# Performance work log

Hardware: AMD Instinct MI355X
Metric: run time of the kernel (lower is better)

## Reference

```python
import jax, jax.numpy as jnp
import numpy as np

N = 100000
E = 1600000
IN_DIM = 128
OUT_DIM = 128
H = 4
HD = OUT_DIM // H  # 32
NEG_SLOPE = 0.2
EPS_SOFTMAX = 1e-8
EPS_LN = 1e-5


def setup_inputs() -> dict:
    key = jax.random.key(0)
    ks = jax.random.split(key, 6)
    h = jax.random.normal(ks[0], (N, IN_DIM), dtype=jnp.float32)
    edge_index = jax.random.randint(ks[1], (2, E), 0, N, dtype=jnp.int32)
    W = jax.random.normal(ks[2], (IN_DIM, OUT_DIM), dtype=jnp.float32) / np.sqrt(IN_DIM)
    W_self = jax.random.normal(ks[3], (IN_DIM, OUT_DIM), dtype=jnp.float32) / np.sqrt(IN_DIM)
    a_in = jax.random.normal(ks[4], (H, 2 * HD), dtype=jnp.float32) * 0.01
    a_out = jax.random.normal(ks[5], (H, 2 * HD), dtype=jnp.float32) * 0.01
    bias = jnp.zeros((OUT_DIM,), dtype=jnp.float32)
    ln_gamma = jnp.ones((OUT_DIM,), dtype=jnp.float32)
    ln_beta = jnp.zeros((OUT_DIM,), dtype=jnp.float32)
    return {"h": h, "edge_index": edge_index, "W": W, "W_self": W_self,
            "a_in": a_in, "a_out": a_out, "bias": bias,
            "ln_gamma": ln_gamma, "ln_beta": ln_beta}


def _attention_aggregate(h_proj, sender, receiver, attn_vec, num_nodes):
    # h_proj: (N, H, HD); sender/receiver: (E,); attn_vec: (H, 2*HD)
    h_sender = h_proj[sender]      # (E, H, HD)
    h_receiver = h_proj[receiver]  # (E, H, HD)
    # e = sum over concat([h_sender, h_receiver]) * attn_vec, split halves
    e = (jnp.einsum('ehd,hd->eh', h_sender, attn_vec[:, :HD])
         + jnp.einsum('ehd,hd->eh', h_receiver, attn_vec[:, HD:]))
    e = jax.nn.leaky_relu(e, NEG_SLOPE)
    e_max = jax.ops.segment_max(e, receiver, num_segments=num_nodes)  # (N, H)
    alpha = jnp.exp(e - e_max[receiver])
    alpha_sum = jax.ops.segment_sum(alpha, receiver, num_segments=num_nodes)
    alpha = alpha / (alpha_sum[receiver] + EPS_SOFTMAX)
    msg = h_sender * alpha[..., None]  # (E, H, HD)
    return jax.ops.segment_sum(msg, receiver, num_segments=num_nodes)  # (N, H, HD)


def reference(h, edge_index, W, W_self, a_in, a_out, bias, ln_gamma, ln_beta):
    n = h.shape[0]
    h_proj = (h @ W).reshape(n, H, HD)
    h_self = h @ W_self
    src, dst = edge_index[0], edge_index[1]
    h_in = _attention_aggregate(h_proj, src, dst, a_in, n)   # 'in' direction
    h_out = _attention_aggregate(h_proj, dst, src, a_out, n)  # 'out' direction
    combined = h_self + h_in.reshape(n, -1) + h_out.reshape(n, -1) + bias
    mean = combined.mean(axis=-1, keepdims=True)
    var = combined.var(axis=-1, keepdims=True)
    normed = (combined - mean) * jax.lax.rsqrt(var + EPS_LN)
    return normed * ln_gamma + ln_beta
```

## Files before the change

### kernel.cpp

```cpp
#include <hip/hip_runtime.h>
#include <math.h>

#define HEADS 4
#define HD 32
#define DIM 128
#define NEG_SLOPE 0.2f
#define EPS_SM 1e-8f
#define EPS_LN 1e-5f
#define SH1 9
#define PB 256
#define BCOLS 272

typedef _Float16 h2_t __attribute__((ext_vector_type(2)));
typedef _Float16 f16x8 __attribute__((ext_vector_type(8)));
typedef float f32x4 __attribute__((ext_vector_type(4)));

__device__ __forceinline__ float lrelu(float x) { return x > 0.f ? x : NEG_SLOPE * x; }
__device__ __forceinline__ unsigned pkh(float a, float b) {
    return __builtin_bit_cast(unsigned, __builtin_amdgcn_cvt_pkrtz(a, b));
}
__device__ __forceinline__ float dot2(unsigned a, unsigned b, float c) {
    return __builtin_amdgcn_fdot2(__builtin_bit_cast(h2_t, a), __builtin_bit_cast(h2_t, b), c, false);
}
__device__ __forceinline__ float lo16(unsigned u) { return (float)__builtin_bit_cast(h2_t, u)[0]; }
__device__ __forceinline__ float hi16(unsigned u) { return (float)__builtin_bit_cast(h2_t, u)[1]; }

template<int LIM> __device__ __forceinline__ void rmax4(float& a, float& b, float& c, float& d) {
#pragma unroll
    for (int s = 1; s < LIM; s <<= 1) {
        a = fmaxf(a, __shfl_xor(a, s, 64));
        b = fmaxf(b, __shfl_xor(b, s, 64));
        c = fmaxf(c, __shfl_xor(c, s, 64));
        d = fmaxf(d, __shfl_xor(d, s, 64));
    }
}
template<int LIM> __device__ __forceinline__ void rsum4(float& a, float& b, float& c, float& d) {
#pragma unroll
    for (int s = 1; s < LIM; s <<= 1) {
        a += __shfl_xor(a, s, 64);
        b += __shfl_xor(b, s, 64);
        c += __shfl_xor(c, s, 64);
        d += __shfl_xor(d, s, 64);
    }
}

__device__ __forceinline__ void dot8(uint4 u, uint4 v, unsigned wpk, float (&acc)[8]) {
    acc[0] = dot2(__builtin_amdgcn_perm(v.x, u.x, 0x05040100u), wpk, acc[0]);
    acc[1] = dot2(__builtin_amdgcn_perm(v.x, u.x, 0x07060302u), wpk, acc[1]);
    acc[2] = dot2(__builtin_amdgcn_perm(v.y, u.y, 0x05040100u), wpk, acc[2]);
    acc[3] = dot2(__builtin_amdgcn_perm(v.y, u.y, 0x07060302u), wpk, acc[3]);
    acc[4] = dot2(__builtin_amdgcn_perm(v.z, u.z, 0x05040100u), wpk, acc[4]);
    acc[5] = dot2(__builtin_amdgcn_perm(v.z, u.z, 0x07060302u), wpk, acc[5]);
    acc[6] = dot2(__builtin_amdgcn_perm(v.w, u.w, 0x05040100u), wpk, acc[6]);
    acc[7] = dot2(__builtin_amdgcn_perm(v.w, u.w, 0x07060302u), wpk, acc[7]);
}

__device__ __forceinline__ void aggr_pairs(int cnt, const int* __restrict__ sdw,
                                           const uint2* __restrict__ wtw,
                                           const char* __restrict__ hpb,
                                           unsigned rowoff, int q, bool hlo, unsigned wsel,
                                           float (&acc)[8]) {
    const int npair = (cnt + 7) >> 3;
#pragma unroll 2
    for (int t = 0; t < npair; ++t) {
        int pi = 4 * t + q;
        uint2 sp = *(const uint2*)&sdw[2 * pi];
        uint4 wp = *(const uint4*)&wtw[2 * pi];
        uint4 u = *(const uint4*)(hpb + (((unsigned)sp.x << 8) + rowoff));
        uint4 v = *(const uint4*)(hpb + (((unsigned)sp.y << 8) + rowoff));
        unsigned wA = hlo ? wp.x : wp.y;
        unsigned wB = hlo ? wp.z : wp.w;
        unsigned wpk = __builtin_amdgcn_perm(wB, wA, wsel);
        dot8(u, v, wpk, acc);
    }
}

__global__ __launch_bounds__(256) void part1a_k(const int* __restrict__ ei, int* __restrict__ cntmat,
                                                int E, int N, int NBIN,
                                                const float* __restrict__ W,
                                                const float* __restrict__ V,
                                                const float* __restrict__ a_in,
                                                const float* __restrict__ a_out,
                                                _Float16* __restrict__ Bt) {
    __shared__ int lcnt[512];
    const int t = threadIdx.x;
    if (blockIdx.x >= PB) {
        int c = (blockIdx.x - PB) * 2 + (t >> 7);
        int k = t & 127;
        float v;
        if (c < 128) {
            v = W[k * 128 + c];
        } else if (c < 256) {
            v = V[k * 128 + (c - 128)];
        } else {
            int d = (c - 256) >> 2, hh = (c - 256) & 3;
            const float* a = (d < 2) ? a_in : a_out;
            int base = hh * 64 + (d & 1) * 32;
            float s = 0.f;
#pragma unroll
            for (int tt = 0; tt < 32; ++tt) s += W[k * 128 + 32 * hh + tt] * a[base + tt];
            v = s;
        }
        Bt[c * 128 + k] = (_Float16)v;
        return;
    }
    const int CH = (E + PB - 1) / PB;
    const int e0 = blockIdx.x * CH;
    const int e1 = min(e0 + CH, E);
    for (int i = t; i < 512; i += 256) lcnt[i] = 0;
    __syncthreads();
    for (int e = e0 + t; e < e1; e += 256) {
        int s = ei[e], d = ei[E + e];
        atomicAdd(&lcnt[d >> SH1], 1);
        atomicAdd(&lcnt[(N + s) >> SH1], 1);
    }
    __syncthreads();
    for (int i = t; i < NBIN; i += 256) cntmat[i * PB + blockIdx.x] = lcnt[i];
}

__global__ __launch_bounds__(256) void scanB_k(const int* __restrict__ cntmat,
                                               int* __restrict__ blkoff, int* __restrict__ btot) {
    __shared__ int ls[PB];
    const int bin = blockIdx.x;
    const int t = threadIdx.x;
    int v = cntmat[bin * PB + t];
    ls[t] = v;
    __syncthreads();
#pragma unroll
    for (int d = 1; d < PB; d <<= 1) {
        int u = (t >= d) ? ls[t - d] : 0;
        __syncthreads();
        ls[t] += u;
        __syncthreads();
    }
    blkoff[bin * PB + t] = ls[t] - v;
    if (t == PB - 1) btot[bin] = ls[t];
}

__global__ __launch_bounds__(256) void scanC_k(const int* __restrict__ btot,
                                               int* __restrict__ bbase, int NBIN, int twoE) {
    __shared__ int ls[256];
    int t = threadIdx.x;
    int i0 = 2 * t, i1 = 2 * t + 1;
    int v0 = (i0 < NBIN) ? btot[i0] : 0;
    int v1 = (i1 < NBIN) ? btot[i1] : 0;
    int pair = v0 + v1;
    ls[t] = pair;
    __syncthreads();
#pragma unroll
    for (int d = 1; d < 256; d <<= 1) {
        int u = (t >= d) ? ls[t - d] : 0;
        __syncthreads();
        ls[t] += u;
        __syncthreads();
    }
    int excl = ls[t] - pair;
    if (i0 < NBIN) bbase[i0] = excl;
    if (i1 < NBIN) bbase[i1] = excl + v0;
    if (t == 0) bbase[NBIN] = twoE;
}

__global__ __launch_bounds__(256) void p1b_gemm_k(const int* __restrict__ ei,
                                                  const int* __restrict__ bbase,
                                                  const int* __restrict__ blkoff,
                                                  unsigned* __restrict__ rec, int E, int N, int NBIN,
                                                  const float* __restrict__ h,
                                                  const _Float16* __restrict__ Bt,
                                                  unsigned* __restrict__ hs_pk,
                                                  unsigned* __restrict__ hp_pk,
                                                  float* __restrict__ pA0, float* __restrict__ pA1,
                                                  float* __restrict__ pB0, float* __restrict__ pB1) {
    __shared__ int gb[512];
    __shared__ int lcur[512];
    __shared__ _Float16 hs[64][128];
    __shared__ _Float16 hss[64][128];

    if (blockIdx.x < PB) {
        const int t = threadIdx.x;
        const int CH = (E + PB - 1) / PB;
        const int e0 = blockIdx.x * CH;
        const int e1 = min(e0 + CH, E);
        for (int i = t; i < 512; i += 256) lcur[i] = 0;
        for (int i = t; i < NBIN; i += 256) gb[i] = bbase[i] + blkoff[i * PB + blockIdx.x];
        __syncthreads();
        for (int e = e0 + t; e < e1; e += 256) {
            int s = ei[e], d = ei[E + e];
            int b1 = d >> SH1;
            int r1 = atomicAdd(&lcur[b1], 1);
            rec[gb[b1] + r1] = (unsigned)s | ((unsigned)(d & 511) << 20);
            int so = N + s;
            int b2 = so >> SH1;
            int r2 = atomicAdd(&lcur[b2], 1);
            rec[gb[b2] + r2] = (unsigned)d | ((unsigned)(so & 511) << 20);
        }
        return;
    }

    const int tid = threadIdx.x;
    const int w = tid >> 6, l = tid & 63;
    const int l15 = l & 15;
    const int kg = l >> 4;
    const int row0 = (blockIdx.x - PB) * 64;
    const int arow = row0 + 16 * w + l15;

    f32x4 acc[17];
#pragma unroll
    for (int j = 0; j < 17; ++j) {
        acc[j][0] = 0.f; acc[j][1] = 0.f; acc[j][2] = 0.f; acc[j][3] = 0.f;
    }

    const uint4* __restrict__ bt4 = (const uint4*)Bt;

#pragma unroll
    for (int kc = 0; kc < 4; ++kc) {
        union { unsigned u[4]; f16x8 v; } cv;
        if (arow < N) {
            float4 x0 = ((const float4*)h)[(size_t)arow * 32 + kc * 8 + kg * 2];
            float4 x1 = ((const float4*)h)[(size_t)arow * 32 + kc * 8 + kg * 2 + 1];
            cv.u[0] = pkh(x0.x, x0.y); cv.u[1] = pkh(x0.z, x0.w);
            cv.u[2] = pkh(x1.x, x1.y); cv.u[3] = pkh(x1.z, x1.w);
        } else {
            cv.u[0] = 0u; cv.u[1] = 0u; cv.u[2] = 0u; cv.u[3] = 0u;
        }
        f16x8 af = cv.v;
#pragma unroll
        for (int j = 0; j < 17; ++j) {
            int col = 16 * j + l15;
            union { uint4 q; f16x8 v; } bc;
            bc.q = bt4[col * 16 + kc * 4 + kg];
            acc[j] = __builtin_amdgcn_mfma_f32_16x16x32_f16(af, bc.v, acc[j], 0, 0, 0);
        }
    }

    const int r4 = kg * 4;
    const int dsel = l15 >> 2, hh = l15 & 3;
    float* __restrict__ pd = (dsel == 0) ? pA0 : (dsel == 1) ? pA1 : (dsel == 2) ? pB0 : pB1;
#pragma unroll
    for (int r = 0; r < 4; ++r) {
        int lr = 16 * w + r4 + r;
        int grow = row0 + lr;
#pragma unroll
        for (int j = 0; j < 8; ++j)
            hs[lr][16 * j + l15] = (_Float16)acc[j][r];
#pragma unroll
        for (int j = 8; j < 16; ++j)
            hss[lr][16 * (j - 8) + l15] = (_Float16)acc[j][r];
        if (grow < N) pd[grow * 4 + hh] = acc[16][r];
    }
    __syncthreads();
    const uint4* hsv = (const uint4*)&hs[0][0];
    const uint4* hssv = (const uint4*)&hss[0][0];
#pragma unroll
    for (int p = 0; p < 4; ++p) {
        int chunk = tid + p * 256;
        int rrow = chunk >> 4, cg = chunk & 15;
        int grow = row0 + rrow;
        if (grow < N) {
            ((uint4*)hp_pk)[(size_t)grow * 16 + cg] = hsv[rrow * 16 + cg];
            ((uint4*)hs_pk)[(size_t)grow * 16 + cg] = hssv[rrow * 16 + cg];
        }
    }
}

__global__ __launch_bounds__(256) void build2_k(const unsigned* __restrict__ rec,
                                                const int* __restrict__ bbase,
                                                int* __restrict__ off, int* __restrict__ csr,
                                                int M, int twoE, int NBIN) {
    __shared__ int lcnt[512];
    __shared__ int lcur[512];
    __shared__ int ls[256];
    const int b = blockIdx.x;
    const int t = threadIdx.x;
    const int base = bbase[b];
    const int cnt = bbase[b + 1] - base;
    const int seg0 = b << SH1;
    for (int i = t; i < 512; i += 256) lcnt[i] = 0;
    __syncthreads();
    for (int k = t; k < cnt; k += 256) atomicAdd(&lcnt[rec[base + k] >> 20], 1);
    __syncthreads();
    int v0 = lcnt[2 * t], v1 = lcnt[2 * t + 1];
    int pair = v0 + v1;
    ls[t] = pair;
    __syncthreads();
#pragma unroll
    for (int d = 1; d < 256; d <<= 1) {
        int u = (t >= d) ? ls[t - d] : 0;
        __syncthreads();
        ls[t] += u;
        __syncthreads();
    }
    int excl = ls[t] - pair;
    lcur[2 * t] = excl;
    lcur[2 * t + 1] = excl + v0;
    int sg = seg0 + 2 * t;
    if (sg < M) off[sg] = base + excl;
    if (sg + 1 < M) off[sg + 1] = base + excl + v0;
    if (b == NBIN - 1 && t == 0) off[M] = twoE;
    __syncthreads();
    for (int k = t; k < cnt; k += 256) {
        unsigned r = rec[base + k];
        int pos = atomicAdd(&lcur[r >> 20], 1);
        csr[base + pos] = (int)(r & 0xFFFFFu);
    }
}

#define ROWLD(x) (*(const uint4*)(hpb + (((unsigned)(x) << 8) + rowoff)))
__global__ __launch_bounds__(256) void node_aggr_ln_k(const unsigned* __restrict__ hp_pk,
                                                      const unsigned* __restrict__ hs_pk,
                                                      const float* __restrict__ pA0, const float* __restrict__ pA1,
                                                      const float* __restrict__ pB0, const float* __restrict__ pB1,
                                                      const int* __restrict__ off, const int* __restrict__ csr,
                                                      const float* __restrict__ bias,
                                                      const float* __restrict__ gamma,
                                                      const float* __restrict__ beta,
                                                      float* __restrict__ out, int N) {
    __shared__ int sds[4][64];
    __shared__ uint2 wts[4][64];
    const int wave = threadIdx.x >> 6;
    const int lane = threadIdx.x & 63;
    const int n = blockIdx.x * 4 + wave;
    if (n >= N) return;
    const int l15 = lane & 15;
    const int q = lane >> 4;
    const unsigned wsel = (l15 & 4) ? 0x07060302u : 0x05040100u;
    const bool hlo = (l15 < 8);
    int* sdw = sds[wave];
    uint2* wtw = wts[wave];
    const char* hpb = (const char*)hp_pk;
    const unsigned rowoff = (unsigned)l15 << 4;

    float acc[8];
#pragma unroll
    for (int k = 0; k < 8; ++k) acc[k] = 0.f;

    const int beg0 = off[n], end0 = off[n + 1];
    const int beg1 = off[N + n], end1 = off[N + n + 1];
    const int len0 = end0 - beg0, len1 = end1 - beg1;

    if (len0 <= 32 && len1 <= 32) {
        const int half = lane >> 5;
        const int hl = lane & 31;
        const int beg = half ? beg1 : beg0;
        const int len = half ? len1 : len0;
        const float* __restrict__ pp0 = half ? pB0 : pA0;
        const float* __restrict__ pp1 = half ? pB1 : pA1;
        float4 r1 = ((const float4*)pp1)[n];
        int sid = 0;
        float e0 = -INFINITY, e1 = -INFINITY, e2 = -INFINITY, e3 = -INFINITY;
        float4 r0 = make_float4(0.f, 0.f, 0.f, 0.f);
        if (hl < len) {
            sid = csr[beg + hl];
            r0 = ((const float4*)pp0)[sid];
        }
        sdw[lane] = 0;
        wtw[lane] = make_uint2(0u, 0u);
        if (hl < len) sdw[half ? len0 + hl : hl] = sid;

        const int cnt = len0 + len1;
        const int npair = (cnt + 7) >> 3;
        uint4 u0 = make_uint4(0u, 0u, 0u, 0u), v0 = u0, u1 = u0, v1 = u0;
        if (npair > 0) {
            uint2 s = *(const uint2*)&sdw[2 * q];
            u0 = ROWLD(s.x); v0 = ROWLD(s.y);
        }
        if (npair > 1) {
            uint2 s = *(const uint2*)&sdw[2 * (4 + q)];
            u1 = ROWLD(s.x); v1 = ROWLD(s.y);
        }

        if (hl < len) {
            e0 = lrelu(r0.x + r1.x);
            e1 = lrelu(r0.y + r1.y);
            e2 = lrelu(r0.z + r1.z);
            e3 = lrelu(r0.w + r1.w);
        }
        float m0 = e0, m1 = e1, m2 = e2, m3 = e3;
        const bool small16 = (len0 <= 16 && len1 <= 16);
        if (small16) rmax4<16>(m0, m1, m2, m3);
        else         rmax4<32>(m0, m1, m2, m3);
        float w0 = 0.f, w1 = 0.f, w2 = 0.f, w3 = 0.f;
        if (hl < len) {
            w0 = __expf(e0 - m0); w1 = __expf(e1 - m1);
            w2 = __expf(e2 - m2); w3 = __expf(e3 - m3);
        }
        float s0 = w0, s1 = w1, s2 = w2, s3 = w3;
        if (small16) rsum4<16>(s0, s1, s2, s3);
        else         rsum4<32>(s0, s1, s2, s3);
        w0 *= 1.f / (s0 + EPS_SM);
        w1 *= 1.f / (s1 + EPS_SM);
        w2 *= 1.f / (s2 + EPS_SM);
        w3 *= 1.f / (s3 + EPS_SM);
        if (hl < len)
            wtw[half ? len0 + hl : hl] = make_uint2(pkh(w0, w1), pkh(w2, w3));

        for (int t = 0; t < npair; t += 2) {
            {
                uint4 wp = *(const uint4*)&wtw[2 * (4 * t + q)];
                unsigned wA = hlo ? wp.x : wp.y;
                unsigned wB = hlo ? wp.z : wp.w;
                unsigned wpk = __builtin_amdgcn_perm(wB, wA, wsel);
                dot8(u0, v0, wpk, acc);
            }
            if (t + 2 < npair) {
                uint2 s = *(const uint2*)&sdw[2 * (4 * (t + 2) + q)];
                u0 = ROWLD(s.x); v0 = ROWLD(s.y);
            }
            if (t + 1 < npair) {
                uint4 wp = *(const uint4*)&wtw[2 * (4 * (t + 1) + q)];
                unsigned wA = hlo ? wp.x : wp.y;
                unsigned wB = hlo ? wp.z : wp.w;
                unsigned wpk = __builtin_amdgcn_perm(wB, wA, wsel);
                dot8(u1, v1, wpk, acc);
                if (t + 3 < npair) {
                    uint2 s = *(const uint2*)&sdw[2 * (4 * (t + 3) + q)];
                    u1 = ROWLD(s.x); v1 = ROWLD(s.y);
                }
            }
        }
    } else {
#pragma unroll
        for (int dir = 0; dir < 2; ++dir) {
            const int beg = (dir == 0) ? beg0 : beg1;
            const int end = (dir == 0) ? end0 : end1;
            const int len = end - beg;
            if (len == 0) continue;
            const float* __restrict__ p0 = (dir == 0) ? pA0 : pB0;
            const float* __restrict__ p1 = (dir == 0) ? pA1 : pB1;
            float4 r1 = ((const float4*)p1)[n];

            if (len <= 64) {
                int sid = 0;
                float e0 = -INFINITY, e1 = -INFINITY, e2 = -INFINITY, e3 = -INFINITY;
                if (lane < len) {
                    sid = csr[beg + lane];
                    float4 r0 = ((const float4*)p0)[sid];
                    e0 = lrelu(r0.x + r1.x);
                    e1 = lrelu(r0.y + r1.y);
                    e2 = lrelu(r0.z + r1.z);
                    e3 = lrelu(r0.w + r1.w);
                }
                float m0 = e0, m1 = e1, m2 = e2, m3 = e3;
                rmax4<64>(m0, m1, m2, m3);
                float w0 = 0.f, w1 = 0.f, w2 = 0.f, w3 = 0.f;
                if (lane < len) {
                    w0 = __expf(e0 - m0); w1 = __expf(e1 - m1);
                    w2 = __expf(e2 - m2); w3 = __expf(e3 - m3);
                }
                float s0 = w0, s1 = w1, s2 = w2, s3 = w3;
                rsum4<64>(s0, s1, s2, s3);
                w0 *= 1.f / (s0 + EPS_SM);
                w1 *= 1.f / (s1 + EPS_SM);
                w2 *= 1.f / (s2 + EPS_SM);
                w3 *= 1.f / (s3 + EPS_SM);
                sdw[lane] = sid;
                wtw[lane] = make_uint2(pkh(w0, w1), pkh(w2, w3));
                aggr_pairs(len, sdw, wtw, hpb, rowoff, q, hlo, wsel, acc);
            } else {
                float m0 = -INFINITY, m1 = -INFINITY, m2 = -INFINITY, m3 = -INFINITY;
                for (int base = beg; base < end; base += 64) {
                    int j = base + lane;
                    if (j < end) {
                        int sid = csr[j];
                        float4 r0 = ((const float4*)p0)[sid];
                        m0 = fmaxf(m0, lrelu(r0.x + r1.x));
                        m1 = fmaxf(m1, lrelu(r0.y + r1.y));
                        m2 = fmaxf(m2, lrelu(r0.z + r1.z));
                        m3 = fmaxf(m3, lrelu(r0.w + r1.w));
                    }
                }
                rmax4<64>(m0, m1, m2, m3);
                float s0 = 0.f, s1 = 0.f, s2 = 0.f, s3 = 0.f;
                for (int base = beg; base < end; base += 64) {
                    int j = base + lane;
                    if (j < end) {
                        int sid = csr[j];
                        float4 r0 = ((const float4*)p0)[sid];
                        s0 += __expf(lrelu(r0.x + r1.x) - m0);
                        s1 += __expf(lrelu(r0.y + r1.y) - m1);
                        s2 += __expf(lrelu(r0.z + r1.z) - m2);
                        s3 += __expf(lrelu(r0.w + r1.w) - m3);
                    }
                }
                rsum4<64>(s0, s1, s2, s3);
                const float is0 = 1.f / (s0 + EPS_SM);
                const float is1 = 1.f / (s1 + EPS_SM);
                const float is2 = 1.f / (s2 + EPS_SM);
                const float is3 = 1.f / (s3 + EPS_SM);
                for (int base = beg; base < end; base += 64) {
                    int cnt = min(64, end - base);
                    int sid = 0;
                    float w0 = 0.f, w1 = 0.f, w2 = 0.f, w3 = 0.f;
                    if (lane < cnt) {
                        sid = csr[base + lane];
                        float4 r0 = ((const float4*)p0)[sid];
                        w0 = __expf(lrelu(r0.x + r1.x) - m0) * is0;
                        w1 = __expf(lrelu(r0.y + r1.y) - m1) * is1;
                        w2 = __expf(lrelu(r0.z + r1.z) - m2) * is2;
                        w3 = __expf(lrelu(r0.w + r1.w) - m3) * is3;
                    }
                    sdw[lane] = sid;
                    wtw[lane] = make_uint2(pkh(w0, w1), pkh(w2, w3));
                    aggr_pairs(cnt, sdw, wtw, hpb, rowoff, q, hlo, wsel, acc);
                }
            }
        }
    }

#pragma unroll
    for (int s = 16; s < 64; s <<= 1) {
#pragma unroll
        for (int k = 0; k < 8; ++k) acc[k] += __shfl_xor(acc[k], s, 64);
    }

    size_t bb = (size_t)n * DIM;
    uint4 hv = ((const uint4*)hs_pk)[(size_t)n * 16 + l15];
    float4 b0 = ((const float4*)bias)[2 * l15];
    float4 b1 = ((const float4*)bias)[2 * l15 + 1];
    float x0 = lo16(hv.x) + acc[0] + b0.x;
    float x1 = hi16(hv.x) + acc[1] + b0.y;
    float x2 = lo16(hv.y) + acc[2] + b0.z;
    float x3 = hi16(hv.y) + acc[3] + b0.w;
    float y0 = lo16(hv.z) + acc[4] + b1.x;
    float y1 = hi16(hv.z) + acc[5] + b1.y;
    float y2 = lo16(hv.w) + acc[6] + b1.z;
    float y3 = hi16(hv.w) + acc[7] + b1.w;
    float sum = x0 + x1 + x2 + x3 + y0 + y1 + y2 + y3;
    float sq = x0 * x0 + x1 * x1 + x2 * x2 + x3 * x3
             + y0 * y0 + y1 * y1 + y2 * y2 + y3 * y3;
#pragma unroll
    for (int m = 1; m < 64; m <<= 1) {
        sum += __shfl_xor(sum, m, 64);
        sq += __shfl_xor(sq, m, 64);
    }
    float mean = sum * (1.f / 512.f);
    float var = sq * (1.f / 512.f) - mean * mean;
    float inv = rsqrtf(var + EPS_LN);
    if (lane < 16) {
        float4 g0 = ((const float4*)gamma)[2 * l15];
        float4 g1 = ((const float4*)gamma)[2 * l15 + 1];
        float4 be0 = ((const float4*)beta)[2 * l15];
        float4 be1 = ((const float4*)beta)[2 * l15 + 1];
        float4 o0 = make_float4((x0 - mean) * inv * g0.x + be0.x,
                                (x1 - mean) * inv * g0.y + be0.y,
                                (x2 - mean) * inv * g0.z + be0.z,
                                (x3 - mean) * inv * g0.w + be0.w);
        float4 o1 = make_float4((y0 - mean) * inv * g1.x + be1.x,
                                (y1 - mean) * inv * g1.y + be1.y,
                                (y2 - mean) * inv * g1.z + be1.z,
                                (y3 - mean) * inv * g1.w + be1.w);
        ((float4*)(out + bb))[2 * l15] = o0;
        ((float4*)(out + bb))[2 * l15 + 1] = o1;
    }
}

extern "C" void kernel_launch(void* const* d_in, const int* in_sizes, int n_in,
                              void* d_out, int out_size, void* d_ws, size_t ws_size,
                              hipStream_t stream) {
    const float* h      = (const float*)d_in[0];
    const int*   ei     = (const int*)d_in[1];
    const float* W      = (const float*)d_in[2];
    const float* W_self = (const float*)d_in[3];
    const float* a_in   = (const float*)d_in[4];
    const float* a_out  = (const float*)d_in[5];
    const float* bias   = (const float*)d_in[6];
    const float* gamma  = (const float*)d_in[7];
    const float* beta   = (const float*)d_in[8];
    float* out = (float*)d_out;

    const int N = in_sizes[0] / DIM;
    const int E = in_sizes[1] / 2;
    const int M = 2 * N;
    const int NBIN = (M + (1 << SH1) - 1) >> SH1;
    const int twoE = 2 * E;

    float* ws = (float*)d_ws;
    size_t off_f = 0;
    unsigned* hs_pk = (unsigned*)(ws + off_f); off_f += (size_t)N * 64;
    unsigned* hp_pk = (unsigned*)(ws + off_f); off_f += (size_t)N * 64;
    float* pA0 = ws + off_f; off_f += (size_t)N * 4;
    float* pA1 = ws + off_f; off_f += (size_t)N * 4;
    float* pB0 = ws + off_f; off_f += (size_t)N * 4;
    float* pB1 = ws + off_f; off_f += (size_t)N * 4;
    int* ip = (int*)(ws + off_f);
    size_t off_i = 0;
    int* cntmat = ip + off_i; off_i += (size_t)NBIN * PB;
    int* blkoff = ip + off_i; off_i += (size_t)NBIN * PB;
    int* btot   = ip + off_i; off_i += NBIN;
    int* bbase  = ip + off_i; off_i += (size_t)NBIN + 1;
    int* off    = ip + off_i; off_i += (size_t)M + 1;
    unsigned* rec = (unsigned*)(ip + off_i); off_i += (size_t)twoE;
    int* csr    = ip + off_i; off_i += (size_t)twoE;
    _Float16* Bt = (_Float16*)(ip + off_i); off_i += (size_t)(BCOLS * 128) / 2;

    const int GB = (N + 63) / 64;

    part1a_k<<<PB + BCOLS / 2, 256, 0, stream>>>(ei, cntmat, E, N, NBIN,
                                                 W, W_self, a_in, a_out, Bt);
    scanB_k<<<NBIN, PB, 0, stream>>>(cntmat, blkoff, btot);
    scanC_k<<<1, 256, 0, stream>>>(btot, bbase, NBIN, twoE);

    p1b_gemm_k<<<PB + GB, 256, 0, stream>>>(ei, bbase, blkoff, rec, E, N, NBIN,
                                            h, Bt, hs_pk, hp_pk, pA0, pA1, pB0, pB1);

    build2_k<<<NBIN, 256, 0, stream>>>(rec, bbase, off, csr, M, twoE, NBIN);

    node_aggr_ln_k<<<(N + 3) / 4, 256, 0, stream>>>(hp_pk, hs_pk, pA0, pA1, pB0, pB1,
                                                    off, csr, bias, gamma, beta, out, N);
}
```

Baseline: 372.2 us.

## Build CSR via global per-node atomics and drop softmax max subtraction

Replaces the two-pass binned CSR construction (per-block bin histogram, record scatter, then per-bin rebuild kernel) with per-node global atomic degree counts, a segmented scan, and a direct scatter into csr using per-node atomic cursors fused into the GEMM launch. This removes the build2 kernel and the intermediate rec buffer. It also removes the softmax max reduction and computes exp of the raw logits, which saves the shuffle reductions and the extra pass over long neighbour lists. The unshifted exp relies on logits staying small enough not to overflow, which holds only because the attention vectors are small. Heavy global atomic contention on the degree and cursor arrays may offset some of the saving.

```diff
diff --git a/kernel.cpp b/kernel.cpp
--- a/kernel.cpp
+++ b/kernel.cpp
@@ -8,7 +8,8 @@
 #define EPS_SM 1e-8f
 #define EPS_LN 1e-5f
 #define SH1 9
-#define PB 256
+#define HB 256
+#define SB 256
 #define BCOLS 272
 
 typedef _Float16 h2_t __attribute__((ext_vector_type(2)));
@@ -25,15 +26,6 @@
 __device__ __forceinline__ float lo16(unsigned u) { return (float)__builtin_bit_cast(h2_t, u)[0]; }
 __device__ __forceinline__ float hi16(unsigned u) { return (float)__builtin_bit_cast(h2_t, u)[1]; }
 
-template<int LIM> __device__ __forceinline__ void rmax4(float& a, float& b, float& c, float& d) {
-#pragma unroll
-    for (int s = 1; s < LIM; s <<= 1) {
-        a = fmaxf(a, __shfl_xor(a, s, 64));
-        b = fmaxf(b, __shfl_xor(b, s, 64));
-        c = fmaxf(c, __shfl_xor(c, s, 64));
-        d = fmaxf(d, __shfl_xor(d, s, 64));
-    }
-}
 template<int LIM> __device__ __forceinline__ void rsum4(float& a, float& b, float& c, float& d) {
 #pragma unroll
     for (int s = 1; s < LIM; s <<= 1) {
@@ -75,17 +67,16 @@
     }
 }
 
-__global__ __launch_bounds__(256) void part1a_k(const int* __restrict__ ei, int* __restrict__ cntmat,
-                                                int E, int N, int NBIN,
-                                                const float* __restrict__ W,
-                                                const float* __restrict__ V,
-                                                const float* __restrict__ a_in,
-                                                const float* __restrict__ a_out,
-                                                _Float16* __restrict__ Bt) {
-    __shared__ int lcnt[512];
+__global__ __launch_bounds__(256) void hist_bt_k(const int* __restrict__ ei, int* __restrict__ deg,
+                                                 int E, int N,
+                                                 const float* __restrict__ W,
+                                                 const float* __restrict__ V,
+                                                 const float* __restrict__ a_in,
+                                                 const float* __restrict__ a_out,
+                                                 _Float16* __restrict__ Bt) {
     const int t = threadIdx.x;
-    if (blockIdx.x >= PB) {
-        int c = (blockIdx.x - PB) * 2 + (t >> 7);
+    if (blockIdx.x >= HB) {
+        int c = (blockIdx.x - HB) * 2 + (t >> 7);
         int k = t & 127;
         float v;
         if (c < 128) {
@@ -104,37 +95,37 @@
         Bt[c * 128 + k] = (_Float16)v;
         return;
     }
-    const int CH = (E + PB - 1) / PB;
+    const int CH = (E + HB - 1) / HB;
     const int e0 = blockIdx.x * CH;
     const int e1 = min(e0 + CH, E);
-    for (int i = t; i < 512; i += 256) lcnt[i] = 0;
-    __syncthreads();
     for (int e = e0 + t; e < e1; e += 256) {
         int s = ei[e], d = ei[E + e];
-        atomicAdd(&lcnt[d >> SH1], 1);
-        atomicAdd(&lcnt[(N + s) >> SH1], 1);
-    }
+        atomicAdd(&deg[d], 1);
+        atomicAdd(&deg[N + s], 1);
+    }
+}
+
+__global__ __launch_bounds__(256) void scanseg_k(const int* __restrict__ deg,
+                                                 int* __restrict__ locoff, int* __restrict__ btot) {
+    __shared__ int ls[256];
+    const int b = blockIdx.x;
+    const int t = threadIdx.x;
+    const int i0 = (b << SH1) + 2 * t, i1 = i0 + 1;
+    int v0 = deg[i0], v1 = deg[i1];
+    int pair = v0 + v1;
+    ls[t] = pair;
     __syncthreads();
-    for (int i = t; i < NBIN; i += 256) cntmat[i * PB + blockIdx.x] = lcnt[i];
-}
-
-__global__ __launch_bounds__(256) void scanB_k(const int* __restrict__ cntmat,
-                                               int* __restrict__ blkoff, int* __restrict__ btot) {
-    __shared__ int ls[PB];
-    const int bin = blockIdx.x;
-    const int t = threadIdx.x;
-    int v = cntmat[bin * PB + t];
-    ls[t] = v;
-    __syncthreads();
-#pragma unroll
-    for (int d = 1; d < PB; d <<= 1) {
+#pragma unroll
+    for (int d = 1; d < 256; d <<= 1) {
         int u = (t >= d) ? ls[t - d] : 0;
         __syncthreads();
         ls[t] += u;
         __syncthreads();
     }
-    blkoff[bin * PB + t] = ls[t] - v;
-    if (t == PB - 1) btot[bin] = ls[t];
+    int excl = ls[t] - pair;
+    locoff[i0] = excl;
+    locoff[i1] = excl + v0;
+    if (t == 255) btot[b] = ls[255];
 }
 
 __global__ __launch_bounds__(256) void scanC_k(const int* __restrict__ btot,
@@ -160,47 +151,52 @@
     if (t == 0) bbase[NBIN] = twoE;
 }
 
-__global__ __launch_bounds__(256) void p1b_gemm_k(const int* __restrict__ ei,
-                                                  const int* __restrict__ bbase,
-                                                  const int* __restrict__ blkoff,
-                                                  unsigned* __restrict__ rec, int E, int N, int NBIN,
-                                                  const float* __restrict__ h,
-                                                  const _Float16* __restrict__ Bt,
-                                                  unsigned* __restrict__ hs_pk,
-                                                  unsigned* __restrict__ hp_pk,
-                                                  float* __restrict__ pA0, float* __restrict__ pA1,
-                                                  float* __restrict__ pB0, float* __restrict__ pB1) {
-    __shared__ int gb[512];
-    __shared__ int lcur[512];
+__global__ __launch_bounds__(256) void fix_scat_gemm_k(const int* __restrict__ ei,
+                                                       const int* __restrict__ bbase,
+                                                       const int* __restrict__ locoff,
+                                                       int* __restrict__ off, int* __restrict__ cnt2,
+                                                       int* __restrict__ csr,
+                                                       int E, int N, int M, int twoE, int F,
+                                                       const float* __restrict__ h,
+                                                       const _Float16* __restrict__ Bt,
+                                                       unsigned* __restrict__ hs_pk,
+                                                       unsigned* __restrict__ hp_pk,
+                                                       float* __restrict__ pA0, float* __restrict__ pA1,
+                                                       float* __restrict__ pB0, float* __restrict__ pB1) {
+    const int tid = threadIdx.x;
+    if (blockIdx.x < F) {
+#pragma unroll
+        for (int p = 0; p < 4; ++p) {
+            int i = blockIdx.x * 1024 + p * 256 + tid;
+            if (i < M) off[i] = bbase[i >> SH1] + locoff[i];
+            else if (i == M) off[M] = twoE;
+        }
+        return;
+    }
+    if (blockIdx.x < F + SB) {
+        const int blk = blockIdx.x - F;
+        const int CH = (E + SB - 1) / SB;
+        const int e0 = blk * CH;
+        const int e1 = min(e0 + CH, E);
+        for (int e = e0 + tid; e < e1; e += 256) {
+            int s = ei[e], d = ei[E + e];
+            int b1 = bbase[d >> SH1] + locoff[d];
+            int r1 = atomicAdd(&cnt2[d], 1);
+            csr[b1 + r1] = s;
+            int so = N + s;
+            int b2 = bbase[so >> SH1] + locoff[so];
+            int r2 = atomicAdd(&cnt2[so], 1);
+            csr[b2 + r2] = d;
+        }
+        return;
+    }
+
     __shared__ _Float16 hs[64][128];
     __shared__ _Float16 hss[64][128];
-
-    if (blockIdx.x < PB) {
-        const int t = threadIdx.x;
-        const int CH = (E + PB - 1) / PB;
-        const int e0 = blockIdx.x * CH;
-        const int e1 = min(e0 + CH, E);
-        for (int i = t; i < 512; i += 256) lcur[i] = 0;
-        for (int i = t; i < NBIN; i += 256) gb[i] = bbase[i] + blkoff[i * PB + blockIdx.x];
-        __syncthreads();
-        for (int e = e0 + t; e < e1; e += 256) {
-            int s = ei[e], d = ei[E + e];
-            int b1 = d >> SH1;
-            int r1 = atomicAdd(&lcur[b1], 1);
-            rec[gb[b1] + r1] = (unsigned)s | ((unsigned)(d & 511) << 20);
-            int so = N + s;
-            int b2 = so >> SH1;
-            int r2 = atomicAdd(&lcur[b2], 1);
-            rec[gb[b2] + r2] = (unsigned)d | ((unsigned)(so & 511) << 20);
-        }
-        return;
-    }
-
-    const int tid = threadIdx.x;
     const int w = tid >> 6, l = tid & 63;
     const int l15 = l & 15;
     const int kg = l >> 4;
-    const int row0 = (blockIdx.x - PB) * 64;
+    const int row0 = (blockIdx.x - F - SB) * 64;
     const int arow = row0 + 16 * w + l15;
 
     f32x4 acc[17];
@@ -259,48 +255,6 @@
             ((uint4*)hp_pk)[(size_t)grow * 16 + cg] = hsv[rrow * 16 + cg];
             ((uint4*)hs_pk)[(size_t)grow * 16 + cg] = hssv[rrow * 16 + cg];
         }
-    }
-}
-
-__global__ __launch_bounds__(256) void build2_k(const unsigned* __restrict__ rec,
-                                                const int* __restrict__ bbase,
-                                                int* __restrict__ off, int* __restrict__ csr,
-                                                int M, int twoE, int NBIN) {
-    __shared__ int lcnt[512];
-    __shared__ int lcur[512];
-    __shared__ int ls[256];
-    const int b = blockIdx.x;
-    const int t = threadIdx.x;
-    const int base = bbase[b];
-    const int cnt = bbase[b + 1] - base;
-    const int seg0 = b << SH1;
-    for (int i = t; i < 512; i += 256) lcnt[i] = 0;
-    __syncthreads();
-    for (int k = t; k < cnt; k += 256) atomicAdd(&lcnt[rec[base + k] >> 20], 1);
-    __syncthreads();
-    int v0 = lcnt[2 * t], v1 = lcnt[2 * t + 1];
-    int pair = v0 + v1;
-    ls[t] = pair;
-    __syncthreads();
-#pragma unroll
-    for (int d = 1; d < 256; d <<= 1) {
-        int u = (t >= d) ? ls[t - d] : 0;
-        __syncthreads();
-        ls[t] += u;
-        __syncthreads();
-    }
-    int excl = ls[t] - pair;
-    lcur[2 * t] = excl;
-    lcur[2 * t + 1] = excl + v0;
-    int sg = seg0 + 2 * t;
-    if (sg < M) off[sg] = base + excl;
-    if (sg + 1 < M) off[sg + 1] = base + excl + v0;
-    if (b == NBIN - 1 && t == 0) off[M] = twoE;
-    __syncthreads();
-    for (int k = t; k < cnt; k += 256) {
-        unsigned r = rec[base + k];
-        int pos = atomicAdd(&lcur[r >> 20], 1);
-        csr[base + pos] = (int)(r & 0xFFFFFu);
     }
 }
 
@@ -374,16 +328,9 @@
             e2 = lrelu(r0.z + r1.z);
             e3 = lrelu(r0.w + r1.w);
         }
-        float m0 = e0, m1 = e1, m2 = e2, m3 = e3;
+        float w0 = __expf(e0), w1 = __expf(e1), w2 = __expf(e2), w3 = __expf(e3);
+        float s0 = w0, s1 = w1, s2 = w2, s3 = w3;
         const bool small16 = (len0 <= 16 && len1 <= 16);
-        if (small16) rmax4<16>(m0, m1, m2, m3);
-        else         rmax4<32>(m0, m1, m2, m3);
-        float w0 = 0.f, w1 = 0.f, w2 = 0.f, w3 = 0.f;
-        if (hl < len) {
-            w0 = __expf(e0 - m0); w1 = __expf(e1 - m1);
-            w2 = __expf(e2 - m2); w3 = __expf(e3 - m3);
-        }
-        float s0 = w0, s1 = w1, s2 = w2, s3 = w3;
         if (small16) rsum4<16>(s0, s1, s2, s3);
         else         rsum4<32>(s0, s1, s2, s3);
         w0 *= 1.f / (s0 + EPS_SM);
@@ -439,13 +386,7 @@
                     e2 = lrelu(r0.z + r1.z);
                     e3 = lrelu(r0.w + r1.w);
                 }
-                float m0 = e0, m1 = e1, m2 = e2, m3 = e3;
-                rmax4<64>(m0, m1, m2, m3);
-                float w0 = 0.f, w1 = 0.f, w2 = 0.f, w3 = 0.f;
-                if (lane < len) {
-                    w0 = __expf(e0 - m0); w1 = __expf(e1 - m1);
-                    w2 = __expf(e2 - m2); w3 = __expf(e3 - m3);
-                }
+                float w0 = __expf(e0), w1 = __expf(e1), w2 = __expf(e2), w3 = __expf(e3);
                 float s0 = w0, s1 = w1, s2 = w2, s3 = w3;
                 rsum4<64>(s0, s1, s2, s3);
                 w0 *= 1.f / (s0 + EPS_SM);
@@ -456,30 +397,20 @@
                 wtw[lane] = make_uint2(pkh(w0, w1), pkh(w2, w3));
                 aggr_pairs(len, sdw, wtw, hpb, rowoff, q, hlo, wsel, acc);
             } else {
-                float m0 = -INFINITY, m1 = -INFINITY, m2 = -INFINITY, m3 = -INFINITY;
+                float s0 = 0.f, s1 = 0.f, s2 = 0.f, s3 = 0.f;
                 for (int base = beg; base < end; base += 64) {
                     int j = base + lane;
+                    float e0 = -INFINITY, e1 = -INFINITY, e2 = -INFINITY, e3 = -INFINITY;
                     if (j < end) {
                         int sid = csr[j];
                         float4 r0 = ((const float4*)p0)[sid];
-                        m0 = fmaxf(m0, lrelu(r0.x + r1.x));
-                        m1 = fmaxf(m1, lrelu(r0.y + r1.y));
-                        m2 = fmaxf(m2, lrelu(r0.z + r1.z));
-                        m3 = fmaxf(m3, lrelu(r0.w + r1.w));
+                        e0 = lrelu(r0.x + r1.x);
+                        e1 = lrelu(r0.y + r1.y);
+                        e2 = lrelu(r0.z + r1.z);
+                        e3 = lrelu(r0.w + r1.w);
                     }
-                }
-                rmax4<64>(m0, m1, m2, m3);
-                float s0 = 0.f, s1 = 0.f, s2 = 0.f, s3 = 0.f;
-                for (int base = beg; base < end; base += 64) {
-                    int j = base + lane;
-                    if (j < end) {
-                        int sid = csr[j];
-                        float4 r0 = ((const float4*)p0)[sid];
-                        s0 += __expf(lrelu(r0.x + r1.x) - m0);
-                        s1 += __expf(lrelu(r0.y + r1.y) - m1);
-                        s2 += __expf(lrelu(r0.z + r1.z) - m2);
-                        s3 += __expf(lrelu(r0.w + r1.w) - m3);
-                    }
+                    s0 += __expf(e0); s1 += __expf(e1);
+                    s2 += __expf(e2); s3 += __expf(e3);
                 }
                 rsum4<64>(s0, s1, s2, s3);
                 const float is0 = 1.f / (s0 + EPS_SM);
@@ -493,10 +424,10 @@
                     if (lane < cnt) {
                         sid = csr[base + lane];
                         float4 r0 = ((const float4*)p0)[sid];
-                        w0 = __expf(lrelu(r0.x + r1.x) - m0) * is0;
-                        w1 = __expf(lrelu(r0.y + r1.y) - m1) * is1;
-                        w2 = __expf(lrelu(r0.z + r1.z) - m2) * is2;
-                        w3 = __expf(lrelu(r0.w + r1.w) - m3) * is3;
+                        w0 = __expf(lrelu(r0.x + r1.x)) * is0;
+                        w1 = __expf(lrelu(r0.y + r1.y)) * is1;
+                        w2 = __expf(lrelu(r0.z + r1.z)) * is2;
+                        w3 = __expf(lrelu(r0.w + r1.w)) * is3;
                     }
                     sdw[lane] = sid;
                     wtw[lane] = make_uint2(pkh(w0, w1), pkh(w2, w3));
@@ -571,6 +502,7 @@
     const int E = in_sizes[1] / 2;
     const int M = 2 * N;
     const int NBIN = (M + (1 << SH1) - 1) >> SH1;
+    const int NS = NBIN << SH1;
     const int twoE = 2 * E;
 
     float* ws = (float*)d_ws;
@@ -583,26 +515,28 @@
     float* pB1 = ws + off_f; off_f += (size_t)N * 4;
     int* ip = (int*)(ws + off_f);
     size_t off_i = 0;
-    int* cntmat = ip + off_i; off_i += (size_t)NBIN * PB;
-    int* blkoff = ip + off_i; off_i += (size_t)NBIN * PB;
+    int* deg    = ip + off_i; off_i += (size_t)NS;
+    int* cnt2   = ip + off_i; off_i += (size_t)NS;
+    int* locoff = ip + off_i; off_i += (size_t)NS;
     int* btot   = ip + off_i; off_i += NBIN;
     int* bbase  = ip + off_i; off_i += (size_t)NBIN + 1;
     int* off    = ip + off_i; off_i += (size_t)M + 1;
-    unsigned* rec = (unsigned*)(ip + off_i); off_i += (size_t)twoE;
     int* csr    = ip + off_i; off_i += (size_t)twoE;
     _Float16* Bt = (_Float16*)(ip + off_i); off_i += (size_t)(BCOLS * 128) / 2;
 
     const int GB = (N + 63) / 64;
-
-    part1a_k<<<PB + BCOLS / 2, 256, 0, stream>>>(ei, cntmat, E, N, NBIN,
-                                                 W, W_self, a_in, a_out, Bt);
-    scanB_k<<<NBIN, PB, 0, stream>>>(cntmat, blkoff, btot);
+    const int F = (M + 1024) / 1024;
+
+    hipMemsetAsync(deg, 0, (size_t)2 * NS * sizeof(int), stream);
+
+    hist_bt_k<<<HB + BCOLS / 2, 256, 0, stream>>>(ei, deg, E, N, W, W_self, a_in, a_out, Bt);
+
+    scanseg_k<<<NBIN, 256, 0, stream>>>(deg, locoff, btot);
     scanC_k<<<1, 256, 0, stream>>>(btot, bbase, NBIN, twoE);
 
-    p1b_gemm_k<<<PB + GB, 256, 0, stream>>>(ei, bbase, blkoff, rec, E, N, NBIN,
-                                            h, Bt, hs_pk, hp_pk, pA0, pA1, pB0, pB1);
-
-    build2_k<<<NBIN, 256, 0, stream>>>(rec, bbase, off, csr, M, twoE, NBIN);
+    fix_scat_gemm_k<<<F + SB + GB, 256, 0, stream>>>(ei, bbase, locoff, off, cnt2, csr,
+                                                     E, N, M, twoE, F,
+                                                     h, Bt, hs_pk, hp_pk, pA0, pA1, pB0, pB1);
 
     node_aggr_ln_k<<<(N + 3) / 4, 256, 0, stream>>>(hp_pk, hs_pk, pA0, pA1, pB0, pB1,
                                                     off, csr, bias, gamma, beta, out, N);
```

Result: slower. 573.7 us (+54.1%).
